# Optimization experiments

Hardware: AMD Instinct MI355X
Metric: run time of the kernel (lower is better)

The kernel has to match this reference:

```python
import jax, jax.numpy as jnp
import numpy as np

WINDOW = 64
STRIDE = 4
IMG_H = 512
IMG_W = 512


def _extract_windows(img, W, stride):
    # img: [H, Wd] -> windows [oh*ow, W, W] (row-major over the output grid,
    # matching torch F.unfold ordering)
    H, Wd = img.shape
    oh = (H - W) // stride + 1
    ow = (Wd - W) // stride + 1
    rows = (jnp.arange(oh) * stride)[:, None] + jnp.arange(W)[None, :]   # [oh, W]
    cols = (jnp.arange(ow) * stride)[:, None] + jnp.arange(W)[None, :]   # [ow, W]
    windows = img[rows[:, None, :, None], cols[None, :, None, :]]        # [oh, ow, W, W]
    return windows.reshape(oh * ow, W, W), oh, ow


def setup_inputs() -> dict:
    key = jax.random.key(0)
    X = jax.random.uniform(key, (1, 1, IMG_H, IMG_W), dtype=jnp.float32)
    return {"X": X}


def reference(X):
    W = WINDOW
    stride = STRIDE
    img = X[0, 0]
    windows, oh, ow = _extract_windows(img, W, stride)  # [N, W, W]

    # sizes = 2**arange(log2(W), 1, -1): e.g. W=64 -> [64, 32, 16, 8, 4]
    sizes = (2 ** np.arange(int(np.log2(W)), 1, -1)).astype(np.int64)
    log_sizes = jnp.log(jnp.asarray(sizes, dtype=jnp.float32))  # [S]

    log_db = []
    for s in sizes:
        s = int(s)
        # box partition of each window: [N, W//s, s, W//s, s]
        r = windows.reshape(-1, W // s, s, W // s, s)
        smax = r.max(axis=(2, 4))
        smin = r.min(axis=(2, 4))
        d_b = (smax - smin).sum(axis=(1, 2))  # [N] per-window box-count sum
        log_db.append(jnp.log(d_b))
    log_db = jnp.stack(log_db)  # [S, N]

    # lstsq with a single column (no intercept): slope = <x, y> / <x, x>
    slope = (log_sizes @ log_db) / (log_sizes @ log_sizes)  # [N]
    fd = -slope
    return fd.reshape(1, 1, oh, ow)
```

## Files before the change

kernel.cpp:

```cpp
#include <hip/hip_runtime.h>
#include <math.h>

#define IMG_W 512
#define OW 113
#define N_WIN (113 * 113)

__device__ __forceinline__ float max4(float4 v) { return fmaxf(fmaxf(v.x, v.y), fmaxf(v.z, v.w)); }
__device__ __forceinline__ float min4(float4 v) { return fminf(fminf(v.x, v.y), fminf(v.z, v.w)); }

__global__ __launch_bounds__(256) void fd_kernel(const float* __restrict__ X,
                                                 float* __restrict__ out) {
    const int w  = blockIdx.x;
    const int ti = w / OW;
    const int tj = w - ti * OW;
    const int t  = threadIdx.x;
    const int a  = t >> 4;
    const int b  = t & 15;

    const int row0 = (ti + a) * 4;
    const int col0 = (tj + b) * 4;
    const float* p = X + row0 * IMG_W + col0;
    float4 r0 = *(const float4*)(p);
    float4 r1 = *(const float4*)(p + IMG_W);
    float4 r2 = *(const float4*)(p + 2 * IMG_W);
    float4 r3 = *(const float4*)(p + 3 * IMG_W);

    float mx = fmaxf(fmaxf(max4(r0), max4(r1)), fmaxf(max4(r2), max4(r3)));
    float mn = fminf(fminf(min4(r0), min4(r1)), fminf(min4(r2), min4(r3)));

    __shared__ float smax[16][16], smin[16][16];
    __shared__ float s8max[8][8],  s8min[8][8];
    __shared__ float s16max[4][4], s16min[4][4];
    __shared__ float s32max[2][2], s32min[2][2];
    __shared__ float wsum[4];

    smax[a][b] = mx;
    smin[a][b] = mn;

    float v4 = mx - mn;
    #pragma unroll
    for (int off = 32; off; off >>= 1) v4 += __shfl_down(v4, off, 64);
    const int lane = t & 63, wid = t >> 6;
    if (lane == 0) wsum[wid] = v4;
    __syncthreads();

    float d8 = 0.f;
    if (t < 64) {
        const int a2 = t >> 3, b2 = t & 7;
        float bm = fmaxf(fmaxf(smax[2*a2][2*b2],   smax[2*a2][2*b2+1]),
                         fmaxf(smax[2*a2+1][2*b2], smax[2*a2+1][2*b2+1]));
        float bn = fminf(fminf(smin[2*a2][2*b2],   smin[2*a2][2*b2+1]),
                         fminf(smin[2*a2+1][2*b2], smin[2*a2+1][2*b2+1]));
        s8max[a2][b2] = bm;
        s8min[a2][b2] = bn;
        float v8 = bm - bn;
        #pragma unroll
        for (int off = 32; off; off >>= 1) v8 += __shfl_down(v8, off, 64);
        d8 = v8;
    }
    __syncthreads();

    float d16 = 0.f;
    if (t < 64) {
        float v16 = 0.f;
        if (t < 16) {
            const int a3 = t >> 2, b3 = t & 3;
            float bm = fmaxf(fmaxf(s8max[2*a3][2*b3],   s8max[2*a3][2*b3+1]),
                             fmaxf(s8max[2*a3+1][2*b3], s8max[2*a3+1][2*b3+1]));
            float bn = fminf(fminf(s8min[2*a3][2*b3],   s8min[2*a3][2*b3+1]),
                             fminf(s8min[2*a3+1][2*b3], s8min[2*a3+1][2*b3+1]));
            s16max[a3][b3] = bm;
            s16min[a3][b3] = bn;
            v16 = bm - bn;
        }
        #pragma unroll
        for (int off = 32; off; off >>= 1) v16 += __shfl_down(v16, off, 64);
        d16 = v16;
    }
    __syncthreads();

    float d32 = 0.f;
    if (t < 64) {
        float v32 = 0.f;
        if (t < 4) {
            const int a4 = t >> 1, b4 = t & 1;
            float bm = fmaxf(fmaxf(s16max[2*a4][2*b4],   s16max[2*a4][2*b4+1]),
                             fmaxf(s16max[2*a4+1][2*b4], s16max[2*a4+1][2*b4+1]));
            float bn = fminf(fminf(s16min[2*a4][2*b4],   s16min[2*a4][2*b4+1]),
                             fminf(s16min[2*a4+1][2*b4], s16min[2*a4+1][2*b4+1]));
            s32max[a4][b4] = bm;
            s32min[a4][b4] = bn;
            v32 = bm - bn;
        }
        #pragma unroll
        for (int off = 32; off; off >>= 1) v32 += __shfl_down(v32, off, 64);
        d32 = v32;
    }
    __syncthreads();

    if (t == 0) {
        float bm = fmaxf(fmaxf(s32max[0][0], s32max[0][1]),
                         fmaxf(s32max[1][0], s32max[1][1]));
        float bn = fminf(fminf(s32min[0][0], s32min[0][1]),
                         fminf(s32min[1][0], s32min[1][1]));
        float d64 = bm - bn;
        float d4  = wsum[0] + wsum[1] + wsum[2] + wsum[3];

        const float LN2 = 0.69314718055994530942f;
        float num = 6.f * logf(d64) + 5.f * logf(d32) + 4.f * logf(d16)
                  + 3.f * logf(d8)  + 2.f * logf(d4);
        out[w] = -num / (90.0f * LN2);
    }
}

extern "C" void kernel_launch(void* const* d_in, const int* in_sizes, int n_in,
                              void* d_out, int out_size, void* d_ws, size_t ws_size,
                              hipStream_t stream) {
    const float* X = (const float*)d_in[0];
    float* out = (float*)d_out;
    fd_kernel<<<N_WIN, 256, 0, stream>>>(X, out);
}
```

Baseline: 69.57 us.

## Share box min/max across overlapping windows via a global 4x4-cell pyramid

Replaces the one-block-per-window kernel, which recomputed every box min/max for each of the 12769 overlapping windows, with a two-kernel scheme. The first kernel builds, for every 4-pixel grid cell, the max-minus-min of boxes of size 4, 8, 16, 32 and 64 anchored there. The second kernel, one thread per window, sums strided entries of these tables and applies the log-regression. This removes the heavy redundant reads and reductions at the cost of a workspace round trip, a second launch, and many scattered global reads per thread in the final kernel.

After: 61.23 us. -12.0%, faster.

```diff
diff --git a/kernel.cpp b/kernel.cpp
--- a/kernel.cpp
+++ b/kernel.cpp
@@ -4,113 +4,147 @@
 #define IMG_W 512
 #define OW 113
 #define N_WIN (113 * 113)
+#define LSTRIDE 128
 
-__device__ __forceinline__ float max4(float4 v) { return fmaxf(fmaxf(v.x, v.y), fmaxf(v.z, v.w)); }
-__device__ __forceinline__ float min4(float4 v) { return fminf(fminf(v.x, v.y), fminf(v.z, v.w)); }
+#define OFF4  0
+#define OFF8  16384
+#define OFF16 32768
+#define OFF32 49152
+#define OFF64 65536
 
-__global__ __launch_bounds__(256) void fd_kernel(const float* __restrict__ X,
-                                                 float* __restrict__ out) {
-    const int w  = blockIdx.x;
-    const int ti = w / OW;
-    const int tj = w - ti * OW;
-    const int t  = threadIdx.x;
-    const int a  = t >> 4;
-    const int b  = t & 15;
+__device__ __forceinline__ float max4f(float4 v) { return fmaxf(fmaxf(v.x, v.y), fmaxf(v.z, v.w)); }
+__device__ __forceinline__ float min4f(float4 v) { return fminf(fminf(v.x, v.y), fminf(v.z, v.w)); }
 
-    const int row0 = (ti + a) * 4;
-    const int col0 = (tj + b) * 4;
-    const float* p = X + row0 * IMG_W + col0;
-    float4 r0 = *(const float4*)(p);
-    float4 r1 = *(const float4*)(p + IMG_W);
-    float4 r2 = *(const float4*)(p + 2 * IMG_W);
-    float4 r3 = *(const float4*)(p + 3 * IMG_W);
+__global__ __launch_bounds__(256) void fd_pyramid(const float* __restrict__ X,
+                                                  float* __restrict__ ws) {
+    float* diff4  = ws + OFF4;
+    float* diff8  = ws + OFF8;
+    float* diff16 = ws + OFF16;
+    float* diff32 = ws + OFF32;
+    float* diff64 = ws + OFF64;
 
-    float mx = fmaxf(fmaxf(max4(r0), max4(r1)), fmaxf(max4(r2), max4(r3)));
-    float mn = fminf(fminf(min4(r0), min4(r1)), fminf(min4(r2), min4(r3)));
+    const int bi = blockIdx.x >> 4;
+    const int bj = blockIdx.x & 15;
+    const int r0 = bi * 8, c0 = bj * 8;
+    const int t = threadIdx.x;
 
-    __shared__ float smax[16][16], smin[16][16];
-    __shared__ float s8max[8][8],  s8min[8][8];
-    __shared__ float s16max[4][4], s16min[4][4];
-    __shared__ float s32max[2][2], s32min[2][2];
-    __shared__ float wsum[4];
+    __shared__ float tmax[23][24], tmin[23][24];
+    __shared__ float p8x[22][24],  p8n[22][24];
+    __shared__ float p16x[20][24], p16n[20][24];
+    __shared__ float p32x[16][24], p32n[16][24];
 
-    smax[a][b] = mx;
-    smin[a][b] = mn;
-
-    float v4 = mx - mn;
-    #pragma unroll
-    for (int off = 32; off; off >>= 1) v4 += __shfl_down(v4, off, 64);
-    const int lane = t & 63, wid = t >> 6;
-    if (lane == 0) wsum[wid] = v4;
-    __syncthreads();
-
-    float d8 = 0.f;
-    if (t < 64) {
-        const int a2 = t >> 3, b2 = t & 7;
-        float bm = fmaxf(fmaxf(smax[2*a2][2*b2],   smax[2*a2][2*b2+1]),
-                         fmaxf(smax[2*a2+1][2*b2], smax[2*a2+1][2*b2+1]));
-        float bn = fminf(fminf(smin[2*a2][2*b2],   smin[2*a2][2*b2+1]),
-                         fminf(smin[2*a2+1][2*b2], smin[2*a2+1][2*b2+1]));
-        s8max[a2][b2] = bm;
-        s8min[a2][b2] = bn;
-        float v8 = bm - bn;
-        #pragma unroll
-        for (int off = 32; off; off >>= 1) v8 += __shfl_down(v8, off, 64);
-        d8 = v8;
+    for (int idx = t; idx < 23 * 23; idx += 256) {
+        const int lr = idx / 23, lc = idx - lr * 23;
+        const int gr = min(r0 + lr, 127);
+        const int gc = min(c0 + lc, 127);
+        const float* p = X + (gr * 4) * IMG_W + gc * 4;
+        float4 a = *(const float4*)(p);
+        float4 b = *(const float4*)(p + IMG_W);
+        float4 c = *(const float4*)(p + 2 * IMG_W);
+        float4 d = *(const float4*)(p + 3 * IMG_W);
+        tmax[lr][lc] = fmaxf(fmaxf(max4f(a), max4f(b)), fmaxf(max4f(c), max4f(d)));
+        tmin[lr][lc] = fminf(fminf(min4f(a), min4f(b)), fminf(min4f(c), min4f(d)));
     }
     __syncthreads();
 
-    float d16 = 0.f;
-    if (t < 64) {
-        float v16 = 0.f;
-        if (t < 16) {
-            const int a3 = t >> 2, b3 = t & 3;
-            float bm = fmaxf(fmaxf(s8max[2*a3][2*b3],   s8max[2*a3][2*b3+1]),
-                             fmaxf(s8max[2*a3+1][2*b3], s8max[2*a3+1][2*b3+1]));
-            float bn = fminf(fminf(s8min[2*a3][2*b3],   s8min[2*a3][2*b3+1]),
-                             fminf(s8min[2*a3+1][2*b3], s8min[2*a3+1][2*b3+1]));
-            s16max[a3][b3] = bm;
-            s16min[a3][b3] = bn;
-            v16 = bm - bn;
+    for (int idx = t; idx < 22 * 22; idx += 256) {
+        const int lr = idx / 22, lc = idx - lr * 22;
+        float x = fmaxf(fmaxf(tmax[lr][lc],     tmax[lr][lc + 1]),
+                        fmaxf(tmax[lr + 1][lc], tmax[lr + 1][lc + 1]));
+        float n = fminf(fminf(tmin[lr][lc],     tmin[lr][lc + 1]),
+                        fminf(tmin[lr + 1][lc], tmin[lr + 1][lc + 1]));
+        p8x[lr][lc] = x;
+        p8n[lr][lc] = n;
+        if (lr < 8 && lc < 8) {
+            diff4[(r0 + lr) * LSTRIDE + c0 + lc] = tmax[lr][lc] - tmin[lr][lc];
+            diff8[(r0 + lr) * LSTRIDE + c0 + lc] = x - n;
         }
-        #pragma unroll
-        for (int off = 32; off; off >>= 1) v16 += __shfl_down(v16, off, 64);
-        d16 = v16;
     }
     __syncthreads();
 
-    float d32 = 0.f;
-    if (t < 64) {
-        float v32 = 0.f;
-        if (t < 4) {
-            const int a4 = t >> 1, b4 = t & 1;
-            float bm = fmaxf(fmaxf(s16max[2*a4][2*b4],   s16max[2*a4][2*b4+1]),
-                             fmaxf(s16max[2*a4+1][2*b4], s16max[2*a4+1][2*b4+1]));
-            float bn = fminf(fminf(s16min[2*a4][2*b4],   s16min[2*a4][2*b4+1]),
-                             fminf(s16min[2*a4+1][2*b4], s16min[2*a4+1][2*b4+1]));
-            s32max[a4][b4] = bm;
-            s32min[a4][b4] = bn;
-            v32 = bm - bn;
-        }
-        #pragma unroll
-        for (int off = 32; off; off >>= 1) v32 += __shfl_down(v32, off, 64);
-        d32 = v32;
+    for (int idx = t; idx < 20 * 20; idx += 256) {
+        const int lr = idx / 20, lc = idx - lr * 20;
+        float x = fmaxf(fmaxf(p8x[lr][lc],     p8x[lr][lc + 2]),
+                        fmaxf(p8x[lr + 2][lc], p8x[lr + 2][lc + 2]));
+        float n = fminf(fminf(p8n[lr][lc],     p8n[lr][lc + 2]),
+                        fminf(p8n[lr + 2][lc], p8n[lr + 2][lc + 2]));
+        p16x[lr][lc] = x;
+        p16n[lr][lc] = n;
+        if (lr < 8 && lc < 8)
+            diff16[(r0 + lr) * LSTRIDE + c0 + lc] = x - n;
     }
     __syncthreads();
 
-    if (t == 0) {
-        float bm = fmaxf(fmaxf(s32max[0][0], s32max[0][1]),
-                         fmaxf(s32max[1][0], s32max[1][1]));
-        float bn = fminf(fminf(s32min[0][0], s32min[0][1]),
-                         fminf(s32min[1][0], s32min[1][1]));
-        float d64 = bm - bn;
-        float d4  = wsum[0] + wsum[1] + wsum[2] + wsum[3];
+    for (int idx = t; idx < 16 * 16; idx += 256) {
+        const int lr = idx >> 4, lc = idx & 15;
+        float x = fmaxf(fmaxf(p16x[lr][lc],     p16x[lr][lc + 4]),
+                        fmaxf(p16x[lr + 4][lc], p16x[lr + 4][lc + 4]));
+        float n = fminf(fminf(p16n[lr][lc],     p16n[lr][lc + 4]),
+                        fminf(p16n[lr + 4][lc], p16n[lr + 4][lc + 4]));
+        p32x[lr][lc] = x;
+        p32n[lr][lc] = n;
+        if (lr < 8 && lc < 8)
+            diff32[(r0 + lr) * LSTRIDE + c0 + lc] = x - n;
+    }
+    __syncthreads();
 
-        const float LN2 = 0.69314718055994530942f;
-        float num = 6.f * logf(d64) + 5.f * logf(d32) + 4.f * logf(d16)
-                  + 3.f * logf(d8)  + 2.f * logf(d4);
-        out[w] = -num / (90.0f * LN2);
+    if (t < 64) {
+        const int lr = t >> 3, lc = t & 7;
+        float x = fmaxf(fmaxf(p32x[lr][lc],     p32x[lr][lc + 8]),
+                        fmaxf(p32x[lr + 8][lc], p32x[lr + 8][lc + 8]));
+        float n = fminf(fminf(p32n[lr][lc],     p32n[lr][lc + 8]),
+                        fminf(p32n[lr + 8][lc], p32n[lr + 8][lc + 8]));
+        diff64[(r0 + lr) * LSTRIDE + c0 + lc] = x - n;
     }
+}
+
+__global__ __launch_bounds__(256) void fd_final(const float* __restrict__ ws,
+                                                float* __restrict__ out) {
+    const int w = blockIdx.x * 256 + threadIdx.x;
+    if (w >= N_WIN) return;
+    const int ti = w / OW;
+    const int tj = w - ti * OW;
+
+    const float* diff4  = ws + OFF4;
+    const float* diff8  = ws + OFF8;
+    const float* diff16 = ws + OFF16;
+    const float* diff32 = ws + OFF32;
+    const float* diff64 = ws + OFF64;
+
+    float d4 = 0.f;
+    #pragma unroll
+    for (int a = 0; a < 16; ++a) {
+        const float* row = diff4 + (ti + a) * LSTRIDE + tj;
+        #pragma unroll
+        for (int b = 0; b < 16; ++b) d4 += row[b];
+    }
+    float d8 = 0.f;
+    #pragma unroll
+    for (int a = 0; a < 8; ++a) {
+        const float* row = diff8 + (ti + 2 * a) * LSTRIDE + tj;
+        #pragma unroll
+        for (int b = 0; b < 8; ++b) d8 += row[2 * b];
+    }
+    float d16 = 0.f;
+    #pragma unroll
+    for (int a = 0; a < 4; ++a) {
+        const float* row = diff16 + (ti + 4 * a) * LSTRIDE + tj;
+        #pragma unroll
+        for (int b = 0; b < 4; ++b) d16 += row[4 * b];
+    }
+    float d32 = 0.f;
+    #pragma unroll
+    for (int a = 0; a < 2; ++a) {
+        const float* row = diff32 + (ti + 8 * a) * LSTRIDE + tj;
+        #pragma unroll
+        for (int b = 0; b < 2; ++b) d32 += row[8 * b];
+    }
+    const float d64 = diff64[ti * LSTRIDE + tj];
+
+    const float LN2 = 0.69314718055994530942f;
+    const float num = 6.f * logf(d64) + 5.f * logf(d32) + 4.f * logf(d16)
+                    + 3.f * logf(d8)  + 2.f * logf(d4);
+    out[w] = -num / (90.0f * LN2);
 }
 
 extern "C" void kernel_launch(void* const* d_in, const int* in_sizes, int n_in,
@@ -118,5 +152,7 @@
                               hipStream_t stream) {
     const float* X = (const float*)d_in[0];
     float* out = (float*)d_out;
-    fd_kernel<<<N_WIN, 256, 0, stream>>>(X, out);
+    float* ws = (float*)d_ws;
+    fd_pyramid<<<256, 256, 0, stream>>>(X, ws);
+    fd_final<<<(N_WIN + 255) / 256, 256, 0, stream>>>(ws, out);
 }
```
